# Kernel optimization log

Measured on AMD Instinct MI355X. Metric: run time of the kernel, lower is better.

Reference implementation:

```python
import jax, jax.numpy as jnp
import numpy as np

B, N, DIN, U, K, DEG = 64, 512, 256, 128, 2, 8
BN = B * N
E = BN * DEG
D4 = 4 * U
HEADS = 2


def setup_inputs() -> dict:
    key = jax.random.key(0)
    ks = jax.random.split(key, 24)
    rng = np.random.default_rng(0)
    # block-diagonal batched graph: each of B graphs has N nodes, N*DEG random edges
    src = rng.integers(0, N, size=(B, N * DEG))
    dst = rng.integers(0, N, size=(B, N * DEG))
    off = (np.arange(B) * N)[:, None]
    edge_index = jnp.asarray(np.stack([(src + off).reshape(-1), (dst + off).reshape(-1)]), dtype=jnp.int32)

    def w(k, shape, fan):
        return (jax.random.normal(k, shape, dtype=jnp.float32) / np.sqrt(fan)).astype(jnp.float32)

    gin = (DIN + U) * (K + 1)  # gconv concatenates K+1 hop features of concat([x, h])
    inp = dict(
        x_od=jax.random.normal(ks[0], (BN, DIN), dtype=jnp.float32),
        history=jax.random.normal(ks[1], (BN, DIN), dtype=jnp.float32),
        yesterday=jax.random.normal(ks[2], (BN, DIN), dtype=jnp.float32),
        edge_index=edge_index,
        edge_weight=jax.random.uniform(ks[3], (E,), dtype=jnp.float32),
        W_ru_f=w(ks[4], (gin, 2 * U), gin), b_ru_f=jnp.zeros((2 * U,), jnp.float32),
        W_c_f=w(ks[5], (gin, U), gin), b_c_f=jnp.zeros((U,), jnp.float32),
        W_ru_l=w(ks[6], (gin, 2 * U), gin), b_ru_l=jnp.zeros((2 * U,), jnp.float32),
        W_c_l=w(ks[7], (gin, U), gin), b_c_l=jnp.zeros((U,), jnp.float32),
        W_ru_s=w(ks[8], (gin, 2 * U), gin), b_ru_s=jnp.zeros((2 * U,), jnp.float32),
        W_c_s=w(ks[9], (gin, U), gin), b_c_s=jnp.zeros((U,), jnp.float32),
        W_hd=w(ks[10], (D4, 2 * U), 2 * U), b_hd=jnp.zeros((D4,), jnp.float32),
        W_in=w(ks[11], (3 * D4, D4), D4), b_in=jnp.zeros((3 * D4,), jnp.float32),
        W_out=w(ks[12], (D4, D4), D4), b_out=jnp.zeros((D4,), jnp.float32),
        W_gate=w(ks[13], (U, D4), D4), b_gate=jnp.zeros((U,), jnp.float32),
    )
    return inp


def _gconv(x, src, dst, ew, W, b):
    # K-hop mean-normalized graph convolution over the batched edge list
    num = x.shape[0]
    deg = jnp.maximum(jax.ops.segment_sum(ew, dst, num_segments=num), 1.0)[:, None]
    feats = [x]
    h = x
    for _ in range(K):
        h = jax.ops.segment_sum(h[src] * ew[:, None], dst, num_segments=num) / deg
        feats.append(h)
    return jnp.concatenate(feats, axis=-1) @ W + b


def _ggru(x, h, src, dst, ew, W_ru, b_ru, W_c, b_c):
    ru = jax.nn.sigmoid(_gconv(jnp.concatenate([x, h], -1), src, dst, ew, W_ru, b_ru))
    r, u = jnp.split(ru, 2, axis=-1)
    c = jnp.tanh(_gconv(jnp.concatenate([x, r * h], -1), src, dst, ew, W_c, b_c))
    return u * h + (1.0 - u) * c


def _pos_enc(seq_len, d):
    pos = jnp.arange(seq_len, dtype=jnp.float32)[:, None]
    div = jnp.exp(jnp.arange(0, d, 2, dtype=jnp.float32) * (-jnp.log(10000.0) / d))
    pe = jnp.zeros((seq_len, d), jnp.float32)
    pe = pe.at[:, 0::2].set(jnp.sin(pos * div)).at[:, 1::2].set(jnp.cos(pos * div))
    return pe  # (seq_len, d)


def reference(x_od, history, yesterday, edge_index, edge_weight,
              W_ru_f, b_ru_f, W_c_f, b_c_f,
              W_ru_l, b_ru_l, W_c_l, b_c_l,
              W_ru_s, b_ru_s, W_c_s, b_c_s,
              W_hd, b_hd, W_in, b_in, W_out, b_out, W_gate, b_gate):
    src, dst = edge_index[0], edge_index[1]
    ew = edge_weight
    h0 = jnp.zeros((BN, U), jnp.float32)
    hf = _ggru(x_od, h0, src, dst, ew, W_ru_f, b_ru_f, W_c_f, b_c_f)      # finished branch
    hl = _ggru(history, h0, src, dst, ew, W_ru_l, b_ru_l, W_c_l, b_c_l)  # long-history branch
    hs = _ggru(yesterday, h0, src, dst, ew, W_ru_s, b_ru_s, W_c_s, b_c_s)  # short-history branch
    # hidden fusion: raw view(-1, 2U, N) as in the torch source
    fusion = jnp.concatenate([hs, hl], axis=-1).reshape(B, 2 * U, N)
    uh = jnp.einsum('oc,bcn->bon', W_hd, fusion) + b_hd[:, None]  # (B, 4U, N)
    uh = uh + _pos_enc(B, D4)[:, :, None]                          # pos-enc over batch dim, as in source
    x = uh.transpose(2, 0, 1)                                      # (N, B, 4U): seq=N, batch=B
    # multi-head self-attention (torch MultiheadAttention semantics)
    qkv = x @ W_in.T + b_in
    q, k_, v = jnp.split(qkv, 3, axis=-1)
    hd = D4 // HEADS
    qh = q.reshape(N, B, HEADS, hd)
    kh = k_.reshape(N, B, HEADS, hd)
    vh = v.reshape(N, B, HEADS, hd)
    scores = jnp.einsum('sbhd,tbhd->bhst', qh, kh) / jnp.sqrt(jnp.float32(hd))
    attn = jax.nn.softmax(scores, axis=-1)
    ctx = jnp.einsum('bhst,tbhd->sbhd', attn, vh).reshape(N, B, D4)
    attn_out = ctx @ W_out.T + b_out                               # (N, B, 4U)
    gated = jnp.einsum('oc,bcn->bon', W_gate, attn_out.transpose(1, 2, 0)) + b_gate[:, None]  # (B, U, N)
    attn_flat = gated.transpose(0, 2, 1).reshape(BN, U)
    # (enc_first_out==finished_hidden, long_hidden, short_hidden, gated attention)
    return jnp.stack([hf, hl, hs, attn_flat])
```

## Files before the change

### kernel.cpp

```cpp
#include <hip/hip_runtime.h>
#include <hip/hip_bf16.h>
#include <math.h>


#define DEV __device__ __forceinline__

typedef __attribute__((ext_vector_type(4))) float  f32x4;
typedef __attribute__((ext_vector_type(4))) float  fvec4;
typedef __attribute__((ext_vector_type(8))) short  bf16x8;
typedef __attribute__((ext_vector_type(4))) unsigned short u16x4;

constexpr int BN_ = 32768;
constexpr int E_  = 262144;
constexpr long OUTSEC = 4194304;
constexpr long ZSZE = 25165824;

DEV unsigned short f2bf(float f){
  union { float f; unsigned u; } v; v.f = f;
  unsigned r = (v.u + 0x7FFFu + ((v.u >> 16) & 1u)) >> 16;
  return (unsigned short)r;
}
DEV float b2f(unsigned short h){
  union { unsigned u; float f; } v; v.u = ((unsigned)h) << 16;
  return v.f;
}

__global__ __launch_bounds__(256) void histdeg_kernel(const int* __restrict__ ei,
    const float* __restrict__ ew, unsigned* __restrict__ cnt, float* __restrict__ deg){
  int e = blockIdx.x*256 + threadIdx.x;
  int d = ei[E_ + e];
  atomicAdd(&cnt[d], 1u);
  atomicAdd(&deg[d], ew[e]);
}

__global__ __launch_bounds__(1024) void scan_kernel(const unsigned* __restrict__ cnt,
                                                    unsigned* __restrict__ rowptr){
  __shared__ unsigned sm[1024];
  __shared__ unsigned carry;
  int tid = threadIdx.x;
  if (tid == 0) carry = 0;
  __syncthreads();
  for (int base = 0; base < BN_; base += 1024){
    unsigned v = cnt[base + tid];
    sm[tid] = v;
    __syncthreads();
    for (int off = 1; off < 1024; off <<= 1){
      unsigned t = (tid >= off) ? sm[tid - off] : 0u;
      __syncthreads();
      sm[tid] += t;
      __syncthreads();
    }
    rowptr[base + tid] = carry + sm[tid] - v;
    __syncthreads();
    if (tid == 1023) carry += sm[1023];
    __syncthreads();
  }
  if (tid == 0) rowptr[BN_] = carry;
}

__global__ __launch_bounds__(256) void scatter_kernel(const int* __restrict__ ei,
    const float* __restrict__ ew, const unsigned* __restrict__ rowptr,
    unsigned* __restrict__ curs, unsigned* __restrict__ csrc, float* __restrict__ csrw){
  int e = blockIdx.x*256 + threadIdx.x;
  int d = ei[E_ + e];
  unsigned pos = atomicAdd(&curs[d], 1u);
  unsigned idx = rowptr[d] + pos;
  csrc[idx] = (unsigned)ei[e];
  csrw[idx] = ew[e];
}

template<int SRC>
__global__ __launch_bounds__(256) void prop3_kernel(const float* __restrict__ x0,
    const float* __restrict__ x1, const float* __restrict__ x2,
    unsigned short* __restrict__ zcat,
    const unsigned* __restrict__ rowptr, const unsigned* __restrict__ csrc,
    const float* __restrict__ csrw, const float* __restrict__ deg){
  int node = blockIdx.x*4 + (threadIdx.x >> 6);
  int l = threadIdx.x & 63;
  int z = blockIdx.z;
  const float* xf = (z == 0) ? x0 : (z == 1) ? x1 : x2;
  const unsigned short* zin = zcat + z*ZSZE + 256;
  unsigned short* zout = zcat + z*ZSZE + (SRC == 0 ? 256 : 512);
  unsigned b0 = rowptr[node], b1 = rowptr[node + 1];
  float a0 = 0.f, a1 = 0.f, a2 = 0.f, a3 = 0.f;
  for (unsigned e = b0; e < b1; ++e){
    int s = csrc[e]; float w = csrw[e];
    if constexpr (SRC == 0){
      fvec4 v = *(const fvec4*)(xf + (long)s*256 + l*4);
      a0 += w*v[0]; a1 += w*v[1]; a2 += w*v[2]; a3 += w*v[3];
    } else {
      u16x4 v = *(const u16x4*)(zin + (long)s*768 + l*4);
      a0 += w*b2f(v[0]); a1 += w*b2f(v[1]); a2 += w*b2f(v[2]); a3 += w*b2f(v[3]);
    }
  }
  float dg = deg[node]; dg = dg > 1.f ? dg : 1.f;
  float inv = 1.f / dg;
  u16x4 o = { f2bf(a0*inv), f2bf(a1*inv), f2bf(a2*inv), f2bf(a3*inv) };
  *(u16x4*)(zout + (long)node*768 + l*4) = o;
}

__global__ __launch_bounds__(256) void convx3_kernel(const float* __restrict__ x0,
    const float* __restrict__ x1, const float* __restrict__ x2,
    unsigned short* __restrict__ zcat){
  int id = blockIdx.x*256 + threadIdx.x;
  int z = blockIdx.z;
  const float* xf = (z == 0) ? x0 : (z == 1) ? x1 : x2;
  fvec4 v = ((const fvec4*)xf)[id];
  int m = id >> 6, c4 = id & 63;
  u16x4 o = { f2bf(v[0]), f2bf(v[1]), f2bf(v[2]), f2bf(v[3]) };
  *(u16x4*)(zcat + z*ZSZE + (long)m*768 + c4*4) = o;
}

__global__ __launch_bounds__(256) void cvt_f2b_kernel(const float* __restrict__ s,
                                                      unsigned short* __restrict__ d, int n){
  int i = blockIdx.x*256 + threadIdx.x;
  if (i < n) d[i] = f2bf(s[i]);
}

__global__ __launch_bounds__(256) void tcvt_kernel(const float* __restrict__ s,
    unsigned short* __restrict__ d, int lgC, int R){
  int id = blockIdx.x*256 + threadIdx.x;
  int r = id >> lgC, c = id & ((1 << lgC) - 1);
  d[(long)c*R + r] = f2bf(s[id]);
}

__global__ __launch_bounds__(256) void weff_kernel(const float* __restrict__ Wru,
    const float* __restrict__ bru, const float* __restrict__ Wc, const float* __restrict__ bc,
    unsigned short* __restrict__ Weff, float* __restrict__ beff){
  int id = blockIdx.x*256 + threadIdx.x;
  int n = id / 768, k = id % 768;
  int row = (k >> 8)*384 + (k & 255);
  int j = n >> 1;
  float w = ((n & 1) == 0) ? Wru[(long)row*256 + 128 + j] : Wc[(long)row*128 + j];
  Weff[(long)n*768 + k] = f2bf(w);
  if (k == 0) beff[n] = ((n & 1) == 0) ? bru[128 + j] : bc[j];
}

__global__ __launch_bounds__(256) void pe_kernel(const float* __restrict__ bhd,
                                                 float* __restrict__ PET4){
  int id = blockIdx.x*256 + threadIdx.x;
  int b = id >> 9, o = id & 511;
  float j2 = (float)(o & ~1);
  float ang = (float)b * expf(-j2 * (9.210340371976184f / 512.f));
  float v = ((o & 1) ? cosf(ang) : sinf(ang)) + bhd[o];
  PET4[(o >> 2)*256 + b*4 + (o & 3)] = v;
}

__global__ __launch_bounds__(256) void peq2_kernel(const float* __restrict__ Win,
    const float* __restrict__ bin, const float* __restrict__ PET4, float* __restrict__ peq2){
  int j = blockIdx.x*4 + (threadIdx.x >> 6);
  int l = threadIdx.x & 63;
  float acc = 0.f;
  for (int o4 = 0; o4 < 128; ++o4){
    fvec4 wv = *(const fvec4*)(Win + (long)j*512 + o4*4);
    fvec4 pv = *(const fvec4*)(PET4 + o4*256 + l*4);
    acc += wv[0]*pv[0] + wv[1]*pv[1] + wv[2]*pv[2] + wv[3]*pv[3];
  }
  peq2[(long)l*1536 + j] = bin[j] + acc;
}

__global__ __launch_bounds__(128) void beq_kernel(const float* __restrict__ Wgt,
    const float* __restrict__ bout, const float* __restrict__ bgate, float* __restrict__ beq){
  int g = threadIdx.x;
  float s = bgate[g];
  for (int c = 0; c < 512; ++c) s += Wgt[(long)g*512 + c] * bout[c];
  beq[g] = s;
}

template<int MODE, int EPI>
__global__ __launch_bounds__(256) void gemm_bt(
    const unsigned short* __restrict__ A, const unsigned short* __restrict__ Bt,
    float* __restrict__ Cf, unsigned short* __restrict__ Cb,
    int Ktot, int lda, int ldb, int ldc,
    long sA, long sB, long sC, int g0,
    const float* __restrict__ bias, const float* __restrict__ pe, float scale)
{
  __shared__ unsigned short As[128*64];
  __shared__ unsigned short Bs[128*64];
  const int tid = threadIdx.x;
  long aOff, bOff, cOff;
  if constexpr (MODE == 0 || MODE == 3){
    aOff = blockIdx.z * sA; bOff = blockIdx.z * sB; cOff = blockIdx.z * sC;
  } else if constexpr (MODE == 1){
    int g = g0 + blockIdx.z;
    long base = (long)(g >> 1)*1536 + (long)(g & 1)*256;
    aOff = base; bOff = base + 512; cOff = (long)blockIdx.z * 262144;
  } else {
    int g = g0 + blockIdx.z;
    aOff = (long)blockIdx.z * 262144;
    bOff = (long)g * 131072;
    cOff = (long)g * 256;
  }
  const int bm = blockIdx.y * 128, bn = blockIdx.x * 128;
  const int w = tid >> 6, l = tid & 63;
  const int wr = w >> 1, wc = w & 1;

  const unsigned short* aB[4];
  const unsigned short* bB[4];
  #pragma unroll
  for (int i = 0; i < 4; ++i){
    int c = tid + i*256;
    int row = c >> 3, gg = c & 7;
    aB[i] = A  + aOff + (long)(bm + row)*lda + gg*8;
    bB[i] = Bt + bOff + (long)(bn + row)*ldb + gg*8;
  }

  f32x4 acc[4][4] = {};
  for (int kt = 0; kt < Ktot; kt += 64){
    #pragma unroll
    for (int i = 0; i < 4; ++i){
      __builtin_amdgcn_global_load_lds(
        (const __attribute__((address_space(1))) unsigned int*)(aB[i] + kt),
        (__attribute__((address_space(3))) unsigned int*)&As[(i*256 + w*64)*8], 16, 0, 0);
      __builtin_amdgcn_global_load_lds(
        (const __attribute__((address_space(1))) unsigned int*)(bB[i] + kt),
        (__attribute__((address_space(3))) unsigned int*)&Bs[(i*256 + w*64)*8], 16, 0, 0);
    }
    __syncthreads();
    #pragma unroll
    for (int ks = 0; ks < 2; ++ks){
      bf16x8 aF[4], bF[4];
      #pragma unroll
      for (int mi = 0; mi < 4; ++mi)
        aF[mi] = *(const bf16x8*)(&As[(wr*64 + mi*16 + (l & 15))*64 + ks*32 + (l >> 4)*8]);
      #pragma unroll
      for (int ni = 0; ni < 4; ++ni)
        bF[ni] = *(const bf16x8*)(&Bs[(wc*64 + ni*16 + (l & 15))*64 + ks*32 + (l >> 4)*8]);
      #pragma unroll
      for (int mi = 0; mi < 4; ++mi)
        #pragma unroll
        for (int ni = 0; ni < 4; ++ni)
          acc[mi][ni] = __builtin_amdgcn_mfma_f32_16x16x32_bf16(aF[mi], bF[ni], acc[mi][ni], 0, 0, 0);
    }
    __syncthreads();
  }
  #pragma unroll
  for (int mi = 0; mi < 4; ++mi){
    #pragma unroll
    for (int ni = 0; ni < 4; ++ni){
      int col = bn + wc*64 + ni*16 + (l & 15);
      int row0 = bm + wr*64 + mi*16 + ((l >> 4) << 2);
      #pragma unroll
      for (int j = 0; j < 4; ++j){
        int row = row0 + j;
        float v = acc[mi][ni][j] * scale;
        if (bias){
          if constexpr (MODE == 3) v += bias[(int)blockIdx.z*256 + col];
          else v += bias[col];
        }
        if constexpr (EPI == 5) v += pe[((row & 63) * 1536) + col];
        if constexpr (EPI == 0){
          Cf[cOff + (long)row*ldc + col] = v;
        } else if constexpr (EPI == 4){
          long orow = (long)(row & 63)*512 + (row >> 6);
          Cf[orow*ldc + col] = v;
        } else if constexpr (EPI == 7){
          float other = __shfl_xor(v, 1);
          if (!(l & 1)){
            float uu = 1.f / (1.f + expf(-v));
            Cf[cOff + (long)row*ldc + (col >> 1)] = (1.f - uu) * tanhf(other);
          }
        } else {
          Cb[cOff + (long)row*ldc + col] = f2bf(v);
        }
      }
    }
  }
}

__global__ __launch_bounds__(256) void afus_kernel(const float* __restrict__ out,
                                                   unsigned short* __restrict__ Afus){
  int rc = blockIdx.x, a = blockIdx.y, b = blockIdx.z;
  int c = threadIdx.x;
  const float* hsrc = out + 2*OUTSEC;
  const float* hlrc = out + 1*OUTSEC;
  long rowb = (long)b*512 + 2*c + a;
  #pragma unroll 4
  for (int r0 = 0; r0 < 32; ++r0){
    int r = rc*32 + r0;
    float v = (r < 128) ? hsrc[rowb*128 + r] : hlrc[rowb*128 + (r - 128)];
    long mrow = (long)(a*256 + r)*64 + b;
    Afus[mrow*256 + c] = f2bf(v);
  }
}

__global__ __launch_bounds__(256) void vt_kernel(const unsigned short* __restrict__ qkv,
                                                 unsigned short* __restrict__ vT){
  int g = blockIdx.y; int b = g >> 1, h = g & 1;
  int tt = blockIdx.x & 7, dt = blockIdx.x >> 3;
  __shared__ unsigned short sm[64][65];
  int lrow = threadIdx.x >> 6, lcol = threadIdx.x & 63;
  const unsigned short* src = qkv + (long)b*1536 + 1024 + (long)h*256 + dt*64;
  #pragma unroll
  for (int i = 0; i < 16; ++i){
    int t = tt*64 + lrow + i*4;
    sm[lrow + i*4][lcol] = src[(long)t*98304 + lcol];
  }
  __syncthreads();
  unsigned short* dstp = vT + (long)g*131072 + (long)(dt*64)*512 + tt*64;
  #pragma unroll
  for (int i = 0; i < 16; ++i){
    int d = lrow + i*4;
    dstp[(long)d*512 + lcol] = sm[lcol][d];
  }
}

__global__ __launch_bounds__(256) void smax_kernel(unsigned short* __restrict__ S){
  long row = (long)blockIdx.x*4 + (threadIdx.x >> 6);
  int l = threadIdx.x & 63;
  unsigned short* p = S + row*512 + l*8;
  bf16x8 v = *(const bf16x8*)p;
  float f[8];
  #pragma unroll
  for (int j = 0; j < 8; ++j) f[j] = b2f((unsigned short)v[j]);
  float m = f[0];
  #pragma unroll
  for (int j = 1; j < 8; ++j) m = fmaxf(m, f[j]);
  #pragma unroll
  for (int off = 32; off; off >>= 1) m = fmaxf(m, __shfl_xor(m, off));
  float s = 0.f;
  #pragma unroll
  for (int j = 0; j < 8; ++j){ f[j] = expf(f[j] - m); s += f[j]; }
  #pragma unroll
  for (int off = 32; off; off >>= 1) s += __shfl_xor(s, off);
  float inv = 1.f / s;
  bf16x8 o;
  #pragma unroll
  for (int j = 0; j < 8; ++j) o[j] = (short)f2bf(f[j]*inv);
  *(bf16x8*)p = o;
}

extern "C" void kernel_launch(void* const* d_in, const int* in_sizes, int n_in,
                              void* d_out, int out_size, void* d_ws, size_t ws_size,
                              hipStream_t stream)
{
  (void)in_sizes; (void)n_in; (void)out_size;
  constexpr long MB = 1l << 20;
  if (ws_size < 200*MB) return;

  const float* x0 = (const float*)d_in[0];
  const float* x1 = (const float*)d_in[1];
  const float* x2 = (const float*)d_in[2];
  const int*   ei = (const int*)d_in[3];
  const float* ew = (const float*)d_in[4];
  const float* Wru[3] = {(const float*)d_in[5], (const float*)d_in[9],  (const float*)d_in[13]};
  const float* bru[3] = {(const float*)d_in[6], (const float*)d_in[10], (const float*)d_in[14]};
  const float* Wc[3]  = {(const float*)d_in[7], (const float*)d_in[11], (const float*)d_in[15]};
  const float* bc[3]  = {(const float*)d_in[8], (const float*)d_in[12], (const float*)d_in[16]};
  const float* Whd  = (const float*)d_in[17]; const float* bhd   = (const float*)d_in[18];
  const float* Win  = (const float*)d_in[19]; const float* bin   = (const float*)d_in[20];
  const float* Wout = (const float*)d_in[21]; const float* bout  = (const float*)d_in[22];
  const float* Wgt  = (const float*)d_in[23]; const float* bgate = (const float*)d_in[24];
  float* out = (float*)d_out;
  char* ws = (char*)d_ws;

  float*    deg    = (float*)(ws + 0);
  unsigned* cnt    = (unsigned*)(ws + 131072);
  unsigned* rowptr = (unsigned*)(ws + 262144);
  unsigned* curs   = (unsigned*)(ws + 524288);
  unsigned* csrc   = (unsigned*)(ws + 786432);
  float*    csrw   = (float*)(ws + 1835008);
  unsigned short* Weff = (unsigned short*)(ws + 2883584);
  float*    beff   = (float*)(ws + 4063232);
  float*    beq    = (float*)(ws + 4194304);
  unsigned short* WIN   = (unsigned short*)(ws + 4456448);
  unsigned short* WGTB  = (unsigned short*)(ws + 6029312);
  unsigned short* WHDT  = (unsigned short*)(ws + 6160384);
  unsigned short* WOUTT = (unsigned short*)(ws + 6422528);
  unsigned short* Wq2t  = (unsigned short*)(ws + 6946816);
  unsigned short* Weqt  = (unsigned short*)(ws + 7733248);
  float*    PET4   = (float*)(ws + 7864320);
  float*    PEQ2   = (float*)(ws + 7995392);
  unsigned short* ZCAT3 = (unsigned short*)(ws + 40*MB);
  unsigned short* AFUS  = (unsigned short*)(ws + 8*MB);
  unsigned short* QKV   = (unsigned short*)(ws + 40*MB);
  unsigned short* VT    = (unsigned short*)(ws + 8*MB);
  unsigned short* SCOREB= (unsigned short*)(ws + 136*MB);
  unsigned short* CTX   = (unsigned short*)(ws + 40*MB);

  hipMemsetAsync(deg,  0, 131072, stream);
  hipMemsetAsync(cnt,  0, 131072, stream);
  hipMemsetAsync(curs, 0, 131072, stream);
  histdeg_kernel<<<1024, 256, 0, stream>>>(ei, ew, cnt, deg);
  scan_kernel<<<1, 1024, 0, stream>>>(cnt, rowptr);
  scatter_kernel<<<1024, 256, 0, stream>>>(ei, ew, rowptr, curs, csrc, csrw);

  for (int br = 0; br < 3; ++br)
    weff_kernel<<<768, 256, 0, stream>>>(Wru[br], bru[br], Wc[br], bc[br],
                                         Weff + (long)br*196608, beff + br*256);
  cvt_f2b_kernel<<<3072, 256, 0, stream>>>(Win, WIN,  786432);
  cvt_f2b_kernel<<<256,  256, 0, stream>>>(Wgt, WGTB, 65536);
  tcvt_kernel<<<512,  256, 0, stream>>>(Whd,  WHDT,  8, 512);
  tcvt_kernel<<<1024, 256, 0, stream>>>(Wout, WOUTT, 9, 512);
  pe_kernel<<<128, 256, 0, stream>>>(bhd, PET4);

  gemm_bt<0,2><<<dim3(2,12,1), 256, 0, stream>>>(WIN, WHDT, nullptr, Wq2t,
      512, 512, 512, 256, 0,0,0, 0, nullptr, nullptr, 1.0f);
  gemm_bt<0,2><<<dim3(4,1,1), 256, 0, stream>>>(WGTB, WOUTT, nullptr, Weqt,
      512, 512, 512, 512, 0,0,0, 0, nullptr, nullptr, 1.0f);
  peq2_kernel<<<384, 256, 0, stream>>>(Win, bin, PET4, PEQ2);
  beq_kernel<<<1, 128, 0, stream>>>(Wgt, bout, bgate, beq);

  convx3_kernel<<<dim3(8192,1,3), 256, 0, stream>>>(x0, x1, x2, ZCAT3);
  prop3_kernel<0><<<dim3(8192,1,3), 256, 0, stream>>>(x0, x1, x2, ZCAT3,
                                                      rowptr, csrc, csrw, deg);
  prop3_kernel<1><<<dim3(8192,1,3), 256, 0, stream>>>(x0, x1, x2, ZCAT3,
                                                      rowptr, csrc, csrw, deg);
  gemm_bt<3,7><<<dim3(2,256,3), 256, 0, stream>>>(ZCAT3, Weff, out, nullptr,
      768, 768, 768, 128, ZSZE, 196608, OUTSEC, 0, beff, nullptr, 1.0f);

  afus_kernel<<<dim3(8,2,64), 256, 0, stream>>>(out, AFUS);
  gemm_bt<0,5><<<dim3(12,256,1), 256, 0, stream>>>(AFUS, Wq2t, nullptr, QKV,
      256, 256, 256, 1536, 0,0,0, 0, nullptr, PEQ2, 1.0f);
  vt_kernel<<<dim3(32,128), 256, 0, stream>>>(QKV, VT);

  gemm_bt<1,2><<<dim3(4,4,128), 256, 0, stream>>>(QKV, QKV, nullptr, SCOREB,
      256, 98304, 98304, 512, 0,0,0, 0, nullptr, nullptr, 0.0625f);
  smax_kernel<<<16384, 256, 0, stream>>>(SCOREB);
  gemm_bt<2,2><<<dim3(2,4,128), 256, 0, stream>>>(SCOREB, VT, nullptr, CTX,
      512, 512, 512, 32768, 0,0,0, 0, nullptr, nullptr, 1.0f);

  gemm_bt<0,4><<<dim3(1,256,1), 256, 0, stream>>>(CTX, Weqt, out + 3*OUTSEC, nullptr,
      512, 512, 512, 128, 0,0,0, 0, beq, nullptr, 1.0f);
}
```

Baseline: 993.2 us.

## Double-buffer GEMM LDS tiles, transpose afus via shared memory, merge weff launches

The bf16 MFMA GEMM now uses two LDS buffers, so the global-to-LDS load of the next K tile is issued before the current tile is computed, with one barrier per iteration. The afus transpose kernel stages data in shared memory so both the reads and the bf16 writes are coalesced and vectorised. The three weff launches are merged into one kernel with a grid y dimension. Double buffering doubles LDS use per block to 64KB, which may lower occupancy.

```diff
diff --git a/kernel.cpp b/kernel.cpp
--- a/kernel.cpp
+++ b/kernel.cpp
@@ -124,16 +124,24 @@
   d[(long)c*R + r] = f2bf(s[id]);
 }
 
-__global__ __launch_bounds__(256) void weff_kernel(const float* __restrict__ Wru,
-    const float* __restrict__ bru, const float* __restrict__ Wc, const float* __restrict__ bc,
+__global__ __launch_bounds__(256) void weff3_kernel(
+    const float* __restrict__ Wru0, const float* __restrict__ Wru1, const float* __restrict__ Wru2,
+    const float* __restrict__ bru0, const float* __restrict__ bru1, const float* __restrict__ bru2,
+    const float* __restrict__ Wc0,  const float* __restrict__ Wc1,  const float* __restrict__ Wc2,
+    const float* __restrict__ bc0,  const float* __restrict__ bc1,  const float* __restrict__ bc2,
     unsigned short* __restrict__ Weff, float* __restrict__ beff){
+  int z = blockIdx.y;
+  const float* Wru = (z == 0) ? Wru0 : (z == 1) ? Wru1 : Wru2;
+  const float* bru = (z == 0) ? bru0 : (z == 1) ? bru1 : bru2;
+  const float* Wc  = (z == 0) ? Wc0  : (z == 1) ? Wc1  : Wc2;
+  const float* bc  = (z == 0) ? bc0  : (z == 1) ? bc1  : bc2;
   int id = blockIdx.x*256 + threadIdx.x;
   int n = id / 768, k = id % 768;
   int row = (k >> 8)*384 + (k & 255);
   int j = n >> 1;
   float w = ((n & 1) == 0) ? Wru[(long)row*256 + 128 + j] : Wc[(long)row*128 + j];
-  Weff[(long)n*768 + k] = f2bf(w);
-  if (k == 0) beff[n] = ((n & 1) == 0) ? bru[128 + j] : bc[j];
+  Weff[(long)z*196608 + (long)n*768 + k] = f2bf(w);
+  if (k == 0) beff[z*256 + n] = ((n & 1) == 0) ? bru[128 + j] : bc[j];
 }
 
 __global__ __launch_bounds__(256) void pe_kernel(const float* __restrict__ bhd,
@@ -175,8 +183,8 @@
     long sA, long sB, long sC, int g0,
     const float* __restrict__ bias, const float* __restrict__ pe, float scale)
 {
-  __shared__ unsigned short As[128*64];
-  __shared__ unsigned short Bs[128*64];
+  __shared__ unsigned short As[2][8192];
+  __shared__ unsigned short Bs[2][8192];
   const int tid = threadIdx.x;
   long aOff, bOff, cOff;
   if constexpr (MODE == 0 || MODE == 3){
@@ -206,34 +214,46 @@
   }
 
   f32x4 acc[4][4] = {};
-  for (int kt = 0; kt < Ktot; kt += 64){
+
+  auto stage = [&](int p, int kt){
     #pragma unroll
     for (int i = 0; i < 4; ++i){
       __builtin_amdgcn_global_load_lds(
         (const __attribute__((address_space(1))) unsigned int*)(aB[i] + kt),
-        (__attribute__((address_space(3))) unsigned int*)&As[(i*256 + w*64)*8], 16, 0, 0);
+        (__attribute__((address_space(3))) unsigned int*)&As[p][(i*256 + w*64)*8], 16, 0, 0);
       __builtin_amdgcn_global_load_lds(
         (const __attribute__((address_space(1))) unsigned int*)(bB[i] + kt),
-        (__attribute__((address_space(3))) unsigned int*)&Bs[(i*256 + w*64)*8], 16, 0, 0);
-    }
-    __syncthreads();
+        (__attribute__((address_space(3))) unsigned int*)&Bs[p][(i*256 + w*64)*8], 16, 0, 0);
+    }
+  };
+  auto compute = [&](int p){
     #pragma unroll
     for (int ks = 0; ks < 2; ++ks){
       bf16x8 aF[4], bF[4];
       #pragma unroll
       for (int mi = 0; mi < 4; ++mi)
-        aF[mi] = *(const bf16x8*)(&As[(wr*64 + mi*16 + (l & 15))*64 + ks*32 + (l >> 4)*8]);
+        aF[mi] = *(const bf16x8*)(&As[p][(wr*64 + mi*16 + (l & 15))*64 + ks*32 + (l >> 4)*8]);
       #pragma unroll
       for (int ni = 0; ni < 4; ++ni)
-        bF[ni] = *(const bf16x8*)(&Bs[(wc*64 + ni*16 + (l & 15))*64 + ks*32 + (l >> 4)*8]);
+        bF[ni] = *(const bf16x8*)(&Bs[p][(wc*64 + ni*16 + (l & 15))*64 + ks*32 + (l >> 4)*8]);
       #pragma unroll
       for (int mi = 0; mi < 4; ++mi)
         #pragma unroll
         for (int ni = 0; ni < 4; ++ni)
           acc[mi][ni] = __builtin_amdgcn_mfma_f32_16x16x32_bf16(aF[mi], bF[ni], acc[mi][ni], 0, 0, 0);
     }
-    __syncthreads();
-  }
+  };
+
+  const int nt = Ktot >> 6;
+  stage(0, 0);
+  __syncthreads();
+  for (int t = 0; t < nt - 1; ++t){
+    stage((t + 1) & 1, (t + 1) << 6);
+    compute(t & 1);
+    __syncthreads();
+  }
+  compute((nt - 1) & 1);
+
   #pragma unroll
   for (int mi = 0; mi < 4; ++mi){
     #pragma unroll
@@ -270,17 +290,32 @@
 
 __global__ __launch_bounds__(256) void afus_kernel(const float* __restrict__ out,
                                                    unsigned short* __restrict__ Afus){
-  int rc = blockIdx.x, a = blockIdx.y, b = blockIdx.z;
-  int c = threadIdx.x;
-  const float* hsrc = out + 2*OUTSEC;
-  const float* hlrc = out + 1*OUTSEC;
-  long rowb = (long)b*512 + 2*c + a;
-  #pragma unroll 4
-  for (int r0 = 0; r0 < 32; ++r0){
-    int r = rc*32 + r0;
-    float v = (r < 128) ? hsrc[rowb*128 + r] : hlrc[rowb*128 + (r - 128)];
-    long mrow = (long)(a*256 + r)*64 + b;
-    Afus[mrow*256 + c] = f2bf(v);
+  __shared__ float sm[64][132];
+  int cq = blockIdx.x, a = blockIdx.y, b = blockIdx.z;
+  int tid = threadIdx.x;
+  #pragma unroll
+  for (int half = 0; half < 2; ++half){
+    const float* sec = out + (half ? 1 : 2)*OUTSEC;
+    int cl = tid >> 2, r0 = (tid & 3)*4;
+    long srow = ((long)b*512 + 2*(cq*64 + cl) + a)*128;
+    #pragma unroll
+    for (int it = 0; it < 8; ++it){
+      int r = r0 + it*16;
+      fvec4 v = *(const fvec4*)(sec + srow + r);
+      *(fvec4*)&sm[cl][r] = v;
+    }
+    __syncthreads();
+    int r = tid >> 1;
+    int c0 = (tid & 1)*32;
+    long mrow = ((long)a*256 + half*128 + r)*64 + b;
+    unsigned short* dst = Afus + mrow*256 + cq*64 + c0;
+    #pragma unroll
+    for (int jj = 0; jj < 8; ++jj){
+      int c = c0 + jj*4;
+      u16x4 o = { f2bf(sm[c][r]), f2bf(sm[c+1][r]), f2bf(sm[c+2][r]), f2bf(sm[c+3][r]) };
+      *(u16x4*)(dst + jj*4) = o;
+    }
+    __syncthreads();
   }
 }
 
@@ -343,10 +378,6 @@
   const float* x2 = (const float*)d_in[2];
   const int*   ei = (const int*)d_in[3];
   const float* ew = (const float*)d_in[4];
-  const float* Wru[3] = {(const float*)d_in[5], (const float*)d_in[9],  (const float*)d_in[13]};
-  const float* bru[3] = {(const float*)d_in[6], (const float*)d_in[10], (const float*)d_in[14]};
-  const float* Wc[3]  = {(const float*)d_in[7], (const float*)d_in[11], (const float*)d_in[15]};
-  const float* bc[3]  = {(const float*)d_in[8], (const float*)d_in[12], (const float*)d_in[16]};
   const float* Whd  = (const float*)d_in[17]; const float* bhd   = (const float*)d_in[18];
   const float* Win  = (const float*)d_in[19]; const float* bin   = (const float*)d_in[20];
   const float* Wout = (const float*)d_in[21]; const float* bout  = (const float*)d_in[22];
@@ -385,9 +416,12 @@
   scan_kernel<<<1, 1024, 0, stream>>>(cnt, rowptr);
   scatter_kernel<<<1024, 256, 0, stream>>>(ei, ew, rowptr, curs, csrc, csrw);
 
-  for (int br = 0; br < 3; ++br)
-    weff_kernel<<<768, 256, 0, stream>>>(Wru[br], bru[br], Wc[br], bc[br],
-                                         Weff + (long)br*196608, beff + br*256);
+  weff3_kernel<<<dim3(768,3), 256, 0, stream>>>(
+      (const float*)d_in[5], (const float*)d_in[9],  (const float*)d_in[13],
+      (const float*)d_in[6], (const float*)d_in[10], (const float*)d_in[14],
+      (const float*)d_in[7], (const float*)d_in[11], (const float*)d_in[15],
+      (const float*)d_in[8], (const float*)d_in[12], (const float*)d_in[16],
+      Weff, beff);
   cvt_f2b_kernel<<<3072, 256, 0, stream>>>(Win, WIN,  786432);
   cvt_f2b_kernel<<<256,  256, 0, stream>>>(Wgt, WGTB, 65536);
   tcvt_kernel<<<512,  256, 0, stream>>>(Whd,  WHDT,  8, 512);
@@ -409,7 +443,7 @@
   gemm_bt<3,7><<<dim3(2,256,3), 256, 0, stream>>>(ZCAT3, Weff, out, nullptr,
       768, 768, 768, 128, ZSZE, 196608, OUTSEC, 0, beff, nullptr, 1.0f);
 
-  afus_kernel<<<dim3(8,2,64), 256, 0, stream>>>(out, AFUS);
+  afus_kernel<<<dim3(4,2,64), 256, 0, stream>>>(out, AFUS);
   gemm_bt<0,5><<<dim3(12,256,1), 256, 0, stream>>>(AFUS, Wq2t, nullptr, QKV,
       256, 256, 256, 1536, 0,0,0, 0, nullptr, PEQ2, 1.0f);
   vt_kernel<<<dim3(32,128), 256, 0, stream>>>(QKV, VT);
```

Result: no change. 1.010 ms (+1.7%).
